# Performance work log

Measured on AMD Instinct MI355X. Metric: run time of the kernel, lower is better.

The kernel has to match this reference:

```python
import jax, jax.numpy as jnp
import numpy as np

B, L, DIM, ET, NH, SD, NC = 32, 200, 36, 128, 64, 9, 2


def setup_inputs() -> dict:
    key = jax.random.key(0)
    ks = jax.random.split(key, 16)
    f = jnp.float32
    vals = jax.random.normal(ks[0], (B, L, DIM), f)
    obs = (jax.random.uniform(ks[1], (B, L, DIM)) < 0.7).astype(f)  # 0/1 observation mask
    x = jnp.concatenate([vals, obs], -1)                            # (B, L, 2*DIM)
    time_steps = jnp.sort(jax.random.uniform(ks[2], (B, L)), axis=1)
    static_info = jax.random.normal(ks[3], (B, SD), f)
    query_param = jnp.linspace(0.0, 1.0, ET, dtype=f)               # nn.Parameter(linspace)

    def lin(k, o, i, s):
        return jax.random.normal(k, (o, i), f) * s

    return dict(
        x=x, time_steps=time_steps, static_info=static_info, query_param=query_param,
        periodic_w=lin(ks[4], ET - 1, 1, 1.0), periodic_b=jnp.zeros((ET - 1,), f),
        timelin_w=lin(ks[5], 1, 1, 1.0), timelin_b=jnp.zeros((1,), f),
        qw=lin(ks[6], ET, ET, ET ** -0.5), qb=jnp.zeros((ET,), f),
        kw=lin(ks[7], ET, ET, ET ** -0.5), kb=jnp.zeros((ET,), f),
        ow=lin(ks[8], DIM, 2 * DIM, (2 * DIM) ** -0.5), ob=jnp.zeros((DIM,), f),
        gru_w_ih=lin(ks[9], 3 * NH, DIM, DIM ** -0.5),
        gru_w_hh=lin(ks[10], 3 * NH, NH, NH ** -0.5),
        gru_b_ih=jnp.zeros((3 * NH,), f), gru_b_hh=jnp.zeros((3 * NH,), f),
        st_w=lin(ks[11], 8, SD, SD ** -0.5), st_b=jnp.zeros((8,), f),
        c1_w=lin(ks[12], NH + 8, NH + 8, (NH + 8) ** -0.5), c1_b=jnp.zeros((NH + 8,), f),
        bn_g=jnp.ones((NH + 8,), f), bn_b=jnp.zeros((NH + 8,), f),
        c2_w=lin(ks[13], NC, NH + 8, (NH + 8) ** -0.5), c2_b=jnp.zeros((NC,), f),
        rand_mask=jax.random.randint(ks[14], (B, L), 0, 2, jnp.int32),
    )


def reference(x, time_steps, static_info, query_param, periodic_w, periodic_b,
              timelin_w, timelin_b, qw, qb, kw, kb, ow, ob,
              gru_w_ih, gru_w_hh, gru_b_ih, gru_b_hh, st_w, st_b,
              c1_w, c1_b, bn_g, bn_b, c2_w, c2_b, rand_mask):
    dim = x.shape[-1] // 2
    irr = x[:, :, dim:]                                   # observation mask channels
    temp = rand_mask.astype(x.dtype)[:, :, None]          # random_masking keep-mask
    m_small = irr * temp
    irr2 = jnp.concatenate([irr, irr], -1)                # (B, L, 2*dim)
    m2 = jnp.concatenate([m_small, m_small], -1)

    def time_emb(tt):
        tt = tt[..., None]
        return jnp.concatenate([tt @ timelin_w.T + timelin_b,
                                jnp.sin(tt @ periodic_w.T + periodic_b)], -1)

    key_e = time_emb(time_steps)                          # (B, L, ET)
    query_e = time_emb(query_param[None, :])[0]           # (ET, ET)
    q = query_e @ qw.T + qb                               # num_heads=1 => dk=ET
    k = key_e @ kw.T + kb
    scores = jnp.einsum('qd,bld->bql', q, k) / jnp.sqrt(jnp.asarray(ET, x.dtype))

    def mta(mask):
        # per-channel masked softmax over keys l: (B, Lq, L, 2*dim)
        s5 = jnp.where(mask[:, None, :, :] == 0, jnp.asarray(-1e9, x.dtype),
                       scores[:, :, :, None])
        p = jax.nn.softmax(s5, axis=2)
        o = jnp.einsum('bqld,bld->bqd', p, x)             # (B, Lq, 2*dim)
        return o @ ow.T + ob                              # (B, Lq, dim)

    out_te = mta(irr2)
    out1_te = mta(m2)

    sx = x[:, :, :dim]
    sx_g = jnp.round(jax.nn.sigmoid(jnp.einsum('bld,ble->bde', sx, sx)))
    sout = jax.nn.sigmoid(jnp.einsum('bqd,bqe->bde', out_te, out_te))

    def step(h, xt):  # torch GRU cell, gate order r,z,n
        gi = xt @ gru_w_ih.T + gru_b_ih
        gh = h @ gru_w_hh.T + gru_b_hh
        ir, iz, inn = jnp.split(gi, 3, -1)
        hr, hz, hn = jnp.split(gh, 3, -1)
        r = jax.nn.sigmoid(ir + hr)
        z = jax.nn.sigmoid(iz + hz)
        n = jnp.tanh(inn + r * hn)
        return (1 - z) * n + z * h, None

    h0 = jnp.zeros((x.shape[0], gru_w_hh.shape[1]), x.dtype)
    h_fin, _ = jax.lax.scan(step, h0, jnp.swapaxes(out_te, 0, 1))

    st = static_info @ st_w.T + st_b
    cls_in = jnp.concatenate([h_fin, st], 1)
    z1 = cls_in @ c1_w.T + c1_b
    mu = z1.mean(0)
    var = z1.var(0)                                       # BatchNorm1d (training stats)
    zn = (z1 - mu) / jnp.sqrt(var + 1e-5) * bn_g + bn_b
    zg = jax.nn.gelu(zn, approximate=False)
    logits = zg @ c2_w.T + c2_b
    return (out_te, out1_te, logits, sx_g, sout, query_param)
```

## Files before the change

kernel.cpp:

```cpp
#include <hip/hip_runtime.h>

#define B_   32
#define L_   200
#define DIM_ 36
#define ET_  128
#define NH_  64
#define SD_  9
#define NC_  2

#define O_TE   0
#define O_T1   147456
#define O_LG   294912
#define O_SXG  294976
#define O_SOUT 336448
#define O_QP   377920

typedef __fp16 half_t;
typedef __attribute__((ext_vector_type(2))) __fp16 half2_t;

__device__ __forceinline__ float sigm(float x) { return 1.f / (1.f + expf(-x)); }
__device__ __forceinline__ float fsigm(float x) {
  return __builtin_amdgcn_rcpf(1.f + __expf(-x));
}
__device__ __forceinline__ float ftanh(float x) {
  return 2.f * __builtin_amdgcn_rcpf(1.f + __expf(-2.f * x)) - 1.f;
}
__device__ __forceinline__ half2_t f2h2(float a, float b) {
  return __builtin_amdgcn_cvt_pkrtz(a, b);
}
__device__ __forceinline__ float dot2acc(half2_t w, half2_t h, float acc) {
#if __has_builtin(__builtin_amdgcn_fdot2)
  return __builtin_amdgcn_fdot2(w, h, acc, false);
#else
  return acc + (float)w.x * (float)h.x + (float)w.y * (float)h.y;
#endif
}

__global__ __launch_bounds__(256) void k_pre2(
    const float* __restrict__ qw, const float* __restrict__ kw,
    const float* __restrict__ qb, const float* __restrict__ qp,
    const float* __restrict__ pw, const float* __restrict__ pb,
    const float* __restrict__ tlw, const float* __restrict__ tlb,
    const float* __restrict__ x, float* __restrict__ qm2,
    float* __restrict__ xmean, float* __restrict__ out) {
  int blk = blockIdx.x, t = threadIdx.x;
  if (blk < 128) {
    __shared__ float eq[128];
    __shared__ float uq[128];
    int q = blk;
    if (t < 128) {
      float tt = qp[q];
      eq[t] = (t == 0) ? tt * tlw[0] + tlb[0]
                       : __sinf(tt * pw[t - 1] + pb[t - 1]);
    }
    __syncthreads();
    if (t < 128) {
      const float4* qw4 = (const float4*)(qw + (size_t)t * 128);
      float a = qb[t];
      #pragma unroll 8
      for (int c = 0; c < 32; c++) {
        float4 w = qw4[c];
        a += eq[4 * c] * w.x + eq[4 * c + 1] * w.y +
             eq[4 * c + 2] * w.z + eq[4 * c + 3] * w.w;
      }
      uq[t] = a;
    }
    __syncthreads();
    if (t < 128) {
      float a = 0.f;
      #pragma unroll 8
      for (int i = 0; i < 128; i++) a += uq[i] * kw[i * 128 + t];
      qm2[q * 128 + t] = a * 0.088388347648318447f;
      if (q == 0) out[O_QP + t] = qp[t];
    }
    return;
  }
  int b = blk - 128;
  if (t < 72) {
    float s = 0.f;
    const float* xb = x + (size_t)b * L_ * 72 + t;
    #pragma unroll 8
    for (int l = 0; l < L_; l++) s += xb[(size_t)l * 72];
    xmean[b * 72 + t] = s * (1.0f / L_);
  }
}

__global__ __launch_bounds__(1024, 1) void k_attn(
    const float* __restrict__ qm, const float* __restrict__ ts,
    const float* __restrict__ pw, const float* __restrict__ pb,
    const float* __restrict__ tlw, const float* __restrict__ tlb,
    const float* __restrict__ x, const int* __restrict__ rm,
    const float* __restrict__ xmean, const float* __restrict__ ow,
    const float* __restrict__ ob, float* __restrict__ out) {
  __shared__ __align__(16) char Abuf[103936];
  __shared__ __align__(16) float qs[16][128];
  __shared__ __align__(16) float sc[16][200];
  __shared__ __align__(16) float owsh[DIM_][72];
  float*   ksA  = (float*)Abuf;
  half2_t* wsh2 = (half2_t*)Abuf;
  float*   sums = (float*)(Abuf + 57600);
  float*   ofr  = (float*)(Abuf + 57600 + 36864);

  int b = blockIdx.x >> 3;
  int q0 = (blockIdx.x & 7) << 4;
  int tid = threadIdx.x;

  const float4* qsrc = (const float4*)(qm + q0 * ET_);
  for (int i = tid; i < 16 * 32; i += 1024) ((float4*)qs)[i] = qsrc[i];
  const float4* owsrc = (const float4*)ow;
  for (int i = tid; i < DIM_ * 18; i += 1024) ((float4*)owsh)[i] = owsrc[i];
  {
    float tl_w = tlw[0], tl_b = tlb[0];
    const float* tsb = ts + b * L_;
    for (int i = tid; i < L_ * 128; i += 1024) {
      int l = i >> 7, j = i & 127;
      float t = tsb[l];
      float e = (j == 0) ? t * tl_w + tl_b : __sinf(t * pw[j - 1] + pb[j - 1]);
      int blkj = (j >> 2) ^ ((l >> 2) & 7);
      ksA[(l << 7) + (blkj << 2) + (j & 3)] = e;
    }
  }
  __syncthreads();

  {
    int w = tid >> 6, lg = tid & 63;
    int qp2 = w >> 1;
    int lh = w & 1;
    float acc[2][2];
    #pragma unroll
    for (int i = 0; i < 2; i++)
      #pragma unroll
      for (int j = 0; j < 2; j++) acc[i][j] = 0.f;
    const float4* ks4 = (const float4*)ksA;
    const float4* qs4 = (const float4*)qs;
    int lbase = 100 * lh + 2 * lg;
    int swz0 = (lbase >> 2) & 7;
    int swz1 = ((lbase + 1) >> 2) & 7;
    #pragma unroll 4
    for (int d4 = 0; d4 < 32; d4++) {
      float4 kv[2];
      {
        int l0c = (lbase < 100 * lh + 100) ? lbase : (100 * lh + 99);
        int l1c = (lbase + 1 < 100 * lh + 100) ? lbase + 1 : (100 * lh + 99);
        kv[0] = ks4[(l0c << 5) + (d4 ^ swz0)];
        kv[1] = ks4[(l1c << 5) + (d4 ^ swz1)];
      }
      #pragma unroll
      for (int i = 0; i < 2; i++) {
        float4 qv = qs4[(2 * qp2 + i) * 32 + d4];
        #pragma unroll
        for (int j = 0; j < 2; j++)
          acc[i][j] += qv.x * kv[j].x + qv.y * kv[j].y +
                       qv.z * kv[j].z + qv.w * kv[j].w;
      }
    }
    if (2 * lg < 100) {
      #pragma unroll
      for (int i = 0; i < 2; i++) {
        float2 v = {acc[i][0], acc[i][1]};
        *((float2*)(&sc[2 * qp2 + i][lbase])) = v;
      }
    }
  }
  __syncthreads();

  {
    int qi = tid >> 6, li = tid & 63;
    float m = -1e30f;
    for (int l = li; l < L_; l += 64) m = fmaxf(m, sc[qi][l]);
    #pragma unroll
    for (int off = 32; off >= 1; off >>= 1) m = fmaxf(m, __shfl_xor(m, off));
    for (int l = li; l < L_; l += 64) sc[qi][l] = __expf(sc[qi][l] - m);
  }

  {
    const float2* xb2 = (const float2*)(x + (size_t)b * L_ * 72);
    const int* rmb = rm + b * L_;
    for (int i = tid; i < L_ * 72; i += 1024) {
      int l = i / 72, c2 = i % 72;
      int seg = c2 / 18, fh = c2 % 18;
      float2 v = xb2[l * 36 + fh];
      float2 o = xb2[l * 36 + 18 + fh];
      float rr = (float)rmb[l];
      float w0, w1;
      if (seg == 0)      { w0 = o.x * v.x;      w1 = o.y * v.y; }
      else if (seg == 1) { w0 = o.x;            w1 = o.y; }
      else if (seg == 2) { w0 = o.x * v.x * rr; w1 = o.y * v.y * rr; }
      else               { w0 = o.x * rr;       w1 = o.y * rr; }
      wsh2[l * 72 + c2] = f2h2(w0, w1);
    }
  }
  __syncthreads();

  {
    int quarter = tid >> 8, tt = tid & 255;
    int qi = tt >> 4, li = tt & 15;
    int l0 = quarter * 50;
    float accA[8], accB[8];
    #pragma unroll
    for (int k = 0; k < 8; k++) { accA[k] = 0.f; accB[k] = 0.f; }
    const float4* wA = (const float4*)wsh2;
    #pragma unroll 2
    for (int l = l0; l < l0 + 50; l++) {
      float ev = sc[qi][l];
      float4 wa = wA[l * 18 + li];
      union { float f; half2_t h; } u0, u1, u2, u3;
      u0.f = wa.x; u1.f = wa.y; u2.f = wa.z; u3.f = wa.w;
      accA[0] += ev * (float)u0.h.x; accA[1] += ev * (float)u0.h.y;
      accA[2] += ev * (float)u1.h.x; accA[3] += ev * (float)u1.h.y;
      accA[4] += ev * (float)u2.h.x; accA[5] += ev * (float)u2.h.y;
      accA[6] += ev * (float)u3.h.x; accA[7] += ev * (float)u3.h.y;
      if (li < 2) {
        float4 wb = wA[l * 18 + 16 + li];
        union { float f; half2_t h; } b0, b1, b2, b3;
        b0.f = wb.x; b1.f = wb.y; b2.f = wb.z; b3.f = wb.w;
        accB[0] += ev * (float)b0.h.x; accB[1] += ev * (float)b0.h.y;
        accB[2] += ev * (float)b1.h.x; accB[3] += ev * (float)b1.h.y;
        accB[4] += ev * (float)b2.h.x; accB[5] += ev * (float)b2.h.y;
        accB[6] += ev * (float)b3.h.x; accB[7] += ev * (float)b3.h.y;
      }
    }
    float* sq = sums + quarter * 2304 + qi * 144;
    float4* sA = (float4*)(sq + 8 * li);
    sA[0] = make_float4(accA[0], accA[1], accA[2], accA[3]);
    sA[1] = make_float4(accA[4], accA[5], accA[6], accA[7]);
    if (li < 2) {
      float4* sB = (float4*)(sq + 128 + 8 * li);
      sB[0] = make_float4(accB[0], accB[1], accB[2], accB[3]);
      sB[1] = make_float4(accB[4], accB[5], accB[6], accB[7]);
    }
  }
  __syncthreads();

  const float* xm = xmean + b * 72;
  for (int idx = tid; idx < 16 * DIM_; idx += 1024) {
    int qq = idx / DIM_, j = idx % DIM_;
    const float* s0 = sums + qq * 144;
    const float* s1 = s0 + 2304;
    const float* s2 = s1 + 2304;
    const float* s3 = s2 + 2304;
    float numA = (s0[j] + s1[j]) + (s2[j] + s3[j]);
    float denA = (s0[36 + j] + s1[36 + j]) + (s2[36 + j] + s3[36 + j]);
    float numB = (s0[72 + j] + s1[72 + j]) + (s2[72 + j] + s3[72 + j]);
    float denB = (s0[108 + j] + s1[108 + j]) + (s2[108 + j] + s3[108 + j]);
    float al, ah, bl, bh;
    if (denA > 0.f) { al = numA / denA; ah = 1.f; }
    else            { al = xm[j];       ah = xm[36 + j]; }
    if (denB > 0.f) { bl = numB / denB; bh = 1.f; }
    else            { bl = xm[j];       bh = xm[36 + j]; }
    float* oq = ofr + qq * 144;
    oq[j] = al;      oq[36 + j] = ah;
    oq[72 + j] = bl; oq[108 + j] = bh;
  }
  __syncthreads();

  for (int idx = tid; idx < 16 * 72; idx += 1024) {
    int qq = idx / 72, t = idx % 72;
    int v = t / DIM_, i2 = t % DIM_;
    const float4* o4 = (const float4*)(ofr + qq * 144 + v * 72);
    const float4* w4 = (const float4*)(owsh[i2]);
    float a = ob[i2];
    #pragma unroll
    for (int d4 = 0; d4 < 18; d4++) {
      float4 ov = o4[d4], wv = w4[d4];
      a += ov.x * wv.x + ov.y * wv.y + ov.z * wv.z + ov.w * wv.w;
    }
    size_t off = ((size_t)b * ET_ + q0 + qq) * DIM_ + i2;
    out[(v == 0 ? O_TE : O_T1) + off] = a;
  }
}

__global__ __launch_bounds__(256, 1) void k_sg(
    const float* __restrict__ out_ro, const float* __restrict__ x,
    const float* __restrict__ wih, const float* __restrict__ bih,
    const float* __restrict__ whh, const float* __restrict__ bhh,
    float* __restrict__ hfin, float* __restrict__ out) {
  __shared__ __align__(16) float ote_s[ET_][DIM_];
  __shared__ float gis[ET_][3 * NH_];
  __shared__ __align__(16) half2_t hpk[NH_ / 2];
  int blk = blockIdx.x, t = threadIdx.x;

  if (blk < 32) {
    int b = blk;
    float* sxs = (float*)gis;
    const float4* osrc = (const float4*)(out_ro + O_TE + (size_t)b * ET_ * DIM_);
    for (int idx = t; idx < ET_ * 9; idx += 256)
      ((float4*)&ote_s[0][0])[idx] = osrc[idx];
    const float4* xsrc = (const float4*)(x + (size_t)b * L_ * 72);
    for (int idx = t; idx < L_ * 18; idx += 256) {
      int l = idx / 18, c = idx % 18;
      ((float4*)&sxs[l * 76])[c] = xsrc[idx];
    }
    __syncthreads();
    for (int idx = t; idx < DIM_ * DIM_; idx += 256) {
      int d = idx / DIM_, e = idx % DIM_;
      float s = 0.f;
      #pragma unroll 8
      for (int q = 0; q < ET_; q++) s += ote_s[q][d] * ote_s[q][e];
      out[O_SOUT + (size_t)b * DIM_ * DIM_ + idx] = sigm(s);
    }
    for (int idx = t; idx < DIM_ * DIM_; idx += 256) {
      int d = idx / DIM_, e = idx % DIM_;
      float s = 0.f;
      #pragma unroll 8
      for (int l = 0; l < L_; l++) s += sxs[l * 76 + d] * sxs[l * 76 + e];
      out[O_SXG + (size_t)b * DIM_ * DIM_ + idx] = rintf(sigm(s));
    }
    return;
  }

  int b = blk - 32;
  const float* ote = out_ro + O_TE;
  const float4* osrc = (const float4*)(ote + (size_t)b * ET_ * DIM_);
  for (int idx = t; idx < ET_ * DIM_ / 4; idx += 256)
    ((float4*)&ote_s[0][0])[idx] = osrc[idx];
  __syncthreads();

  if (t < 3 * NH_) {
    float wv[DIM_];
    const float* wrow = wih + (size_t)t * DIM_;
    #pragma unroll
    for (int d = 0; d < DIM_; d++) wv[d] = wrow[d];
    float bi = bih[t] + ((t < 2 * NH_) ? bhh[t] : 0.f);
    for (int q = 0; q < ET_; q++) {
      const float4* xr = (const float4*)ote_s[q];
      float a = bi;
      #pragma unroll
      for (int c = 0; c < 9; c++) {
        float4 xv = xr[c];
        a += xv.x * wv[4 * c] + xv.y * wv[4 * c + 1] +
             xv.z * wv[4 * c + 2] + xv.w * wv[4 * c + 3];
      }
      gis[q][t] = a;
    }
  }
  __syncthreads();
  if (t >= 64) return;

  half2_t wr[32], wz[32], wn[32];
  {
    const float2* r0 = (const float2*)(whh + (size_t)t * NH_);
    const float2* r1 = (const float2*)(whh + (size_t)(NH_ + t) * NH_);
    const float2* r2 = (const float2*)(whh + (size_t)(2 * NH_ + t) * NH_);
    #pragma unroll
    for (int c = 0; c < 32; c++) {
      float2 a = r0[c], bb = r1[c], cc = r2[c];
      wr[c] = f2h2(a.x, a.y);
      wz[c] = f2h2(bb.x, bb.y);
      wn[c] = f2h2(cc.x, cc.y);
    }
  }
  float bh_n = bhh[2 * NH_ + t];

  float h = 0.f;
  ((half_t*)hpk)[t] = (half_t)0.f;
  for (int q = 0; q < ET_; q++) {
    float gi_r = gis[q][t];
    float gi_z = gis[q][NH_ + t];
    float gi_n = gis[q][2 * NH_ + t];
    float ar = 0.f, az = 0.f, an = 0.f;
    const float4* hp4 = (const float4*)hpk;
    #pragma unroll
    for (int c4 = 0; c4 < 8; c4++) {
      float4 hv = hp4[c4];
      union { float f; half2_t h; } u0, u1, u2, u3;
      u0.f = hv.x; u1.f = hv.y; u2.f = hv.z; u3.f = hv.w;
      int c = c4 * 4;
      ar = dot2acc(wr[c + 0], u0.h, ar);
      az = dot2acc(wz[c + 0], u0.h, az);
      an = dot2acc(wn[c + 0], u0.h, an);
      ar = dot2acc(wr[c + 1], u1.h, ar);
      az = dot2acc(wz[c + 1], u1.h, az);
      an = dot2acc(wn[c + 1], u1.h, an);
      ar = dot2acc(wr[c + 2], u2.h, ar);
      az = dot2acc(wz[c + 2], u2.h, az);
      an = dot2acc(wn[c + 2], u2.h, an);
      ar = dot2acc(wr[c + 3], u3.h, ar);
      az = dot2acc(wz[c + 3], u3.h, az);
      an = dot2acc(wn[c + 3], u3.h, an);
    }
    float r = fsigm(gi_r + ar);
    float z = fsigm(gi_z + az);
    float n = ftanh(gi_n + r * (an + bh_n));
    h = n + z * (h - n);
    ((half_t*)hpk)[t] = (half_t)h;
  }
  hfin[b * NH_ + t] = h;
}

__global__ __launch_bounds__(256) void k_cls(
    const float* __restrict__ hfin, const float* __restrict__ si,
    const float* __restrict__ stw, const float* __restrict__ stb,
    const float* __restrict__ c1w, const float* __restrict__ c1b,
    const float* __restrict__ bng, const float* __restrict__ bnb,
    const float* __restrict__ c2w, const float* __restrict__ c2b,
    float* __restrict__ out) {
  __shared__ float cin[B_][72];
  __shared__ float z1[B_][72];
  __shared__ float zg[B_][72];
  int t = threadIdx.x;
  for (int idx = t; idx < B_ * 8; idx += 256) {
    int b = idx / 8, j = idx % 8;
    float acc = stb[j];
    #pragma unroll
    for (int d = 0; d < SD_; d++) acc += si[b * SD_ + d] * stw[j * SD_ + d];
    cin[b][NH_ + j] = acc;
  }
  for (int idx = t; idx < B_ * NH_; idx += 256)
    cin[idx / NH_][idx % NH_] = hfin[idx];
  __syncthreads();
  for (int idx = t; idx < B_ * 72; idx += 256) {
    int b = idx / 72, j = idx % 72;
    float acc = c1b[j];
    #pragma unroll 8
    for (int d = 0; d < 72; d++) acc += cin[b][d] * c1w[j * 72 + d];
    z1[b][j] = acc;
  }
  __syncthreads();
  if (t < 72) {
    float mu = 0.f;
    for (int b = 0; b < B_; b++) mu += z1[b][t];
    mu *= (1.f / B_);
    float vv = 0.f;
    for (int b = 0; b < B_; b++) { float d = z1[b][t] - mu; vv += d * d; }
    vv *= (1.f / B_);
    float inv = 1.f / sqrtf(vv + 1e-5f);
    float g = bng[t], bb = bnb[t];
    for (int b = 0; b < B_; b++) {
      float zn = (z1[b][t] - mu) * inv * g + bb;
      zg[b][t] = 0.5f * zn * (1.f + erff(zn * 0.70710678118654752f));
    }
  }
  __syncthreads();
  for (int idx = t; idx < B_ * NC_; idx += 256) {
    int b = idx / NC_, c = idx % NC_;
    float acc = c2b[c];
    #pragma unroll 8
    for (int d = 0; d < 72; d++) acc += zg[b][d] * c2w[c * 72 + d];
    out[O_LG + idx] = acc;
  }
}

extern "C" void kernel_launch(void* const* d_in, const int* in_sizes, int n_in,
                              void* d_out, int out_size, void* d_ws,
                              size_t ws_size, hipStream_t stream) {
  const float* x    = (const float*)d_in[0];
  const float* ts   = (const float*)d_in[1];
  const float* si   = (const float*)d_in[2];
  const float* qp   = (const float*)d_in[3];
  const float* pw   = (const float*)d_in[4];
  const float* pb   = (const float*)d_in[5];
  const float* tlw  = (const float*)d_in[6];
  const float* tlb  = (const float*)d_in[7];
  const float* qw   = (const float*)d_in[8];
  const float* qb   = (const float*)d_in[9];
  const float* kw   = (const float*)d_in[10];
  const float* ow   = (const float*)d_in[12];
  const float* ob   = (const float*)d_in[13];
  const float* wih  = (const float*)d_in[14];
  const float* whh  = (const float*)d_in[15];
  const float* bih  = (const float*)d_in[16];
  const float* bhh  = (const float*)d_in[17];
  const float* stw  = (const float*)d_in[18];
  const float* stb  = (const float*)d_in[19];
  const float* c1w  = (const float*)d_in[20];
  const float* c1b  = (const float*)d_in[21];
  const float* bng  = (const float*)d_in[22];
  const float* bnb  = (const float*)d_in[23];
  const float* c2w  = (const float*)d_in[24];
  const float* c2b  = (const float*)d_in[25];
  const int*   rm   = (const int*)d_in[26];

  float* out = (float*)d_out;

  float* W = (float*)d_ws;
  float* ws_qm2   = W;
  float* ws_xmean = W + 16384;
  float* ws_hfin  = W + 18688;

  hipLaunchKernelGGL(k_pre2, dim3(160), dim3(256), 0, stream,
                     qw, kw, qb, qp, pw, pb, tlw, tlb, x, ws_qm2, ws_xmean,
                     out);
  hipLaunchKernelGGL(k_attn, dim3(B_ * 8), dim3(1024), 0, stream,
                     ws_qm2, ts, pw, pb, tlw, tlb, x, rm, ws_xmean, ow, ob,
                     out);
  hipLaunchKernelGGL(k_sg, dim3(64), dim3(256), 0, stream,
                     out, x, wih, bih, whh, bhh, ws_hfin, out);
  hipLaunchKernelGGL(k_cls, dim3(1), dim3(256), 0, stream,
                     ws_hfin, si, stw, stb, c1w, c1b, bng, bnb, c2w, c2b,
                     out);
}
```

Baseline: 233.8 us.

## Fuse query projection and x-mean precompute into attention kernel

Removes the separate k_pre2 launch. Each attention block now computes its own 16 query rows (sin embedding, qw projection, kw projection) and the per-batch x mean in shared memory, reusing the sc, owsh and qs buffers as scratch. This saves one kernel launch and the global round trip for qm2 and xmean. In exchange the query projection is recomputed by all 32 batch blocks that share the same q0 slice, and the xmean sums are repeated by 8 blocks per batch.

```diff
diff --git a/kernel.cpp b/kernel.cpp
--- a/kernel.cpp
+++ b/kernel.cpp
@@ -36,62 +36,15 @@
 #endif
 }
 
-__global__ __launch_bounds__(256) void k_pre2(
+__global__ __launch_bounds__(1024, 1) void k_attn(
     const float* __restrict__ qw, const float* __restrict__ kw,
     const float* __restrict__ qb, const float* __restrict__ qp,
-    const float* __restrict__ pw, const float* __restrict__ pb,
-    const float* __restrict__ tlw, const float* __restrict__ tlb,
-    const float* __restrict__ x, float* __restrict__ qm2,
-    float* __restrict__ xmean, float* __restrict__ out) {
-  int blk = blockIdx.x, t = threadIdx.x;
-  if (blk < 128) {
-    __shared__ float eq[128];
-    __shared__ float uq[128];
-    int q = blk;
-    if (t < 128) {
-      float tt = qp[q];
-      eq[t] = (t == 0) ? tt * tlw[0] + tlb[0]
-                       : __sinf(tt * pw[t - 1] + pb[t - 1]);
-    }
-    __syncthreads();
-    if (t < 128) {
-      const float4* qw4 = (const float4*)(qw + (size_t)t * 128);
-      float a = qb[t];
-      #pragma unroll 8
-      for (int c = 0; c < 32; c++) {
-        float4 w = qw4[c];
-        a += eq[4 * c] * w.x + eq[4 * c + 1] * w.y +
-             eq[4 * c + 2] * w.z + eq[4 * c + 3] * w.w;
-      }
-      uq[t] = a;
-    }
-    __syncthreads();
-    if (t < 128) {
-      float a = 0.f;
-      #pragma unroll 8
-      for (int i = 0; i < 128; i++) a += uq[i] * kw[i * 128 + t];
-      qm2[q * 128 + t] = a * 0.088388347648318447f;
-      if (q == 0) out[O_QP + t] = qp[t];
-    }
-    return;
-  }
-  int b = blk - 128;
-  if (t < 72) {
-    float s = 0.f;
-    const float* xb = x + (size_t)b * L_ * 72 + t;
-    #pragma unroll 8
-    for (int l = 0; l < L_; l++) s += xb[(size_t)l * 72];
-    xmean[b * 72 + t] = s * (1.0f / L_);
-  }
-}
-
-__global__ __launch_bounds__(1024, 1) void k_attn(
-    const float* __restrict__ qm, const float* __restrict__ ts,
+    const float* __restrict__ ts,
     const float* __restrict__ pw, const float* __restrict__ pb,
     const float* __restrict__ tlw, const float* __restrict__ tlb,
     const float* __restrict__ x, const int* __restrict__ rm,
-    const float* __restrict__ xmean, const float* __restrict__ ow,
-    const float* __restrict__ ob, float* __restrict__ out) {
+    const float* __restrict__ ow, const float* __restrict__ ob,
+    float* __restrict__ out) {
   __shared__ __align__(16) char Abuf[103936];
   __shared__ __align__(16) float qs[16][128];
   __shared__ __align__(16) float sc[16][200];
@@ -105,8 +58,52 @@
   int q0 = (blockIdx.x & 7) << 4;
   int tid = threadIdx.x;
 
-  const float4* qsrc = (const float4*)(qm + q0 * ET_);
-  for (int i = tid; i < 16 * 32; i += 1024) ((float4*)qs)[i] = qsrc[i];
+  float* eqs = &sc[0][0];
+  float* uqs = &owsh[0][0];
+  for (int i = tid; i < 16 * 128; i += 1024) {
+    int j = i >> 7, c = i & 127;
+    float tt = qp[q0 + j];
+    eqs[i] = (c == 0) ? tt * tlw[0] + tlb[0]
+                      : __sinf(tt * pw[c - 1] + pb[c - 1]);
+  }
+  if (blockIdx.x == 0 && tid < 128) out[O_QP + tid] = qp[tid];
+  __syncthreads();
+
+  {
+    int t = tid & 127, j0 = tid >> 7;
+    const float4* qw4 = (const float4*)(qw + (size_t)t * 128);
+    float a0 = qb[t], a1 = a0;
+    const float* e0 = eqs + j0 * 128;
+    const float* e1 = eqs + (j0 + 8) * 128;
+    #pragma unroll 4
+    for (int c = 0; c < 32; c++) {
+      float4 w = qw4[c];
+      a0 += e0[4 * c] * w.x + e0[4 * c + 1] * w.y +
+            e0[4 * c + 2] * w.z + e0[4 * c + 3] * w.w;
+      a1 += e1[4 * c] * w.x + e1[4 * c + 1] * w.y +
+            e1[4 * c + 2] * w.z + e1[4 * c + 3] * w.w;
+    }
+    uqs[j0 * 128 + t] = a0;
+    uqs[(j0 + 8) * 128 + t] = a1;
+  }
+  __syncthreads();
+
+  {
+    int t = tid & 127, j0 = tid >> 7;
+    float a0 = 0.f, a1 = 0.f;
+    const float* u0 = uqs + j0 * 128;
+    const float* u1 = uqs + (j0 + 8) * 128;
+    #pragma unroll 8
+    for (int i = 0; i < 128; i++) {
+      float kv = kw[i * 128 + t];
+      a0 += u0[i] * kv;
+      a1 += u1[i] * kv;
+    }
+    qs[j0][t]     = a0 * 0.088388347648318447f;
+    qs[j0 + 8][t] = a1 * 0.088388347648318447f;
+  }
+  __syncthreads();
+
   const float4* owsrc = (const float4*)ow;
   for (int i = tid; i < DIM_ * 18; i += 1024) ((float4*)owsh)[i] = owsrc[i];
   {
@@ -189,6 +186,16 @@
       else               { w0 = o.x * rr;       w1 = o.y * rr; }
       wsh2[l * 72 + c2] = f2h2(w0, w1);
     }
+    float* xmp = &qs[0][0];
+    if (tid < 288) {
+      int quarter = tid / 72, d = tid % 72;
+      const float* xb = x + (size_t)b * L_ * 72 + d;
+      float s = 0.f;
+      #pragma unroll
+      for (int l = quarter * 50; l < quarter * 50 + 50; l++)
+        s += xb[(size_t)l * 72];
+      xmp[quarter * 72 + d] = s;
+    }
   }
   __syncthreads();
 
@@ -232,7 +239,7 @@
   }
   __syncthreads();
 
-  const float* xm = xmean + b * 72;
+  const float* xmp = &qs[0][0];
   for (int idx = tid; idx < 16 * DIM_; idx += 1024) {
     int qq = idx / DIM_, j = idx % DIM_;
     const float* s0 = sums + qq * 144;
@@ -243,11 +250,13 @@
     float denA = (s0[36 + j] + s1[36 + j]) + (s2[36 + j] + s3[36 + j]);
     float numB = (s0[72 + j] + s1[72 + j]) + (s2[72 + j] + s3[72 + j]);
     float denB = (s0[108 + j] + s1[108 + j]) + (s2[108 + j] + s3[108 + j]);
+    float xmj  = (xmp[j] + xmp[72 + j] + xmp[144 + j] + xmp[216 + j]) * 0.005f;
+    float xmj2 = (xmp[36 + j] + xmp[108 + j] + xmp[180 + j] + xmp[252 + j]) * 0.005f;
     float al, ah, bl, bh;
     if (denA > 0.f) { al = numA / denA; ah = 1.f; }
-    else            { al = xm[j];       ah = xm[36 + j]; }
+    else            { al = xmj;         ah = xmj2; }
     if (denB > 0.f) { bl = numB / denB; bh = 1.f; }
-    else            { bl = xm[j];       bh = xm[36 + j]; }
+    else            { bl = xmj;         bh = xmj2; }
     float* oq = ofr + qq * 144;
     oq[j] = al;      oq[36 + j] = ah;
     oq[72 + j] = bl; oq[108 + j] = bh;
@@ -474,15 +483,10 @@
   float* out = (float*)d_out;
 
   float* W = (float*)d_ws;
-  float* ws_qm2   = W;
-  float* ws_xmean = W + 16384;
-  float* ws_hfin  = W + 18688;
-
-  hipLaunchKernelGGL(k_pre2, dim3(160), dim3(256), 0, stream,
-                     qw, kw, qb, qp, pw, pb, tlw, tlb, x, ws_qm2, ws_xmean,
-                     out);
+  float* ws_hfin = W;
+
   hipLaunchKernelGGL(k_attn, dim3(B_ * 8), dim3(1024), 0, stream,
-                     ws_qm2, ts, pw, pb, tlw, tlb, x, rm, ws_xmean, ow, ob,
+                     qw, kw, qb, qp, ts, pw, pb, tlw, tlb, x, rm, ow, ob,
                      out);
   hipLaunchKernelGGL(k_sg, dim3(64), dim3(256), 0, stream,
                      out, x, wih, bih, whh, bhh, ws_hfin, out);
```

Result: slower. 242.5 us (+3.7%).
